# Optimization experiments

Measured on AMD Instinct MI355X. Metric: run time of the kernel, lower is better.

The kernel has to match this reference:

```python
import jax, jax.numpy as jnp
import numpy as np

B, H, W, Z = 4, 256, 256, 64
ITERATIONS = 8
EPSILON = 1e-06
CENTER = 6.0  # 7-point Laplacian diagonal


def _stencil(x):
    # x: [B, H, W, Z]; zero (Dirichlet) boundaries via padded shifts
    west = jnp.pad(x[:, :, :-1, :], ((0, 0), (0, 0), (1, 0), (0, 0)))
    east = jnp.pad(x[:, :, 1:, :], ((0, 0), (0, 0), (0, 1), (0, 0)))
    north = jnp.pad(x[:, :-1, :, :], ((0, 0), (1, 0), (0, 0), (0, 0)))
    south = jnp.pad(x[:, 1:, :, :], ((0, 0), (0, 1), (0, 0), (0, 0)))
    bottom = jnp.pad(x[:, :, :, :-1], ((0, 0), (0, 0), (0, 0), (1, 0)))
    top = jnp.pad(x[:, :, :, 1:], ((0, 0), (0, 0), (0, 0), (0, 1)))
    return CENTER * x - west - east - south - north - bottom - top


def _dot(a, b):
    # per-sample dot product, keepdims for scalar broadcast
    return jnp.sum(a * b, axis=(1, 2, 3), keepdims=True)


def setup_inputs() -> dict:
    key = jax.random.key(0)
    k1, k2, k3 = jax.random.split(key, 3)
    shape = (B, H, W, Z)
    return {
        "x": jax.random.normal(k1, shape, dtype=jnp.float32),
        "b": jax.random.normal(k2, shape, dtype=jnp.float32),
        "reference_sol": jax.random.normal(k3, shape, dtype=jnp.float32),
    }


def reference(x, b, reference_sol):
    r = b - _stencil(x)
    p = r
    rho = _dot(r, r)

    def body(carry, _):
        x, r, p, rho = carry
        w = _stencil(p)
        eta = _dot(p, w)
        alpha = rho / (eta + EPSILON)
        x = x + alpha * p
        r = r - alpha * w
        rho_next = _dot(r, r)
        beta = rho_next / (rho + EPSILON)
        p = r + beta * p
        return (x, r, p, rho_next), None

    (x, r, p, rho), _ = jax.lax.scan(body, (x, r, p, rho), None, length=ITERATIONS)

    diff = x - reference_sol
    loss = jnp.mean(diff * diff)
    max_error = jnp.max(jnp.abs(diff))
    residual_norm_sq = jnp.mean(rho)
    return (loss, x, max_error, residual_norm_sq)
```

## Files before the change

### kernel.cpp

```cpp
#include <hip/hip_runtime.h>

#define B_ 4
#define H_ 256
#define W_ 256
#define Z_ 64
#define NB_ (H_*W_*Z_)
#define N_  (B_*NB_)
#define ITER_ 8
#define EPS_ 1e-6f
#define SLOTS_ 64

#define RHO_OFF   0
#define ETA_OFF   ((ITER_+1)*B_*SLOTS_)
#define LOSS_OFF  (ETA_OFF + ITER_*B_*SLOTS_)
#define MAXE_OFF  (LOSS_OFF + SLOTS_)
#define SCAL_FLOATS (MAXE_OFF + SLOTS_)

struct F8 { float4 a, b; };

__device__ __forceinline__ float wsum(float v){
  v += __shfl_xor(v,32); v += __shfl_xor(v,16); v += __shfl_xor(v,8);
  v += __shfl_xor(v,4);  v += __shfl_xor(v,2);  v += __shfl_xor(v,1);
  return v;
}
__device__ __forceinline__ float wmaxr(float v){
  v = fmaxf(v,__shfl_xor(v,32)); v = fmaxf(v,__shfl_xor(v,16));
  v = fmaxf(v,__shfl_xor(v,8));  v = fmaxf(v,__shfl_xor(v,4));
  v = fmaxf(v,__shfl_xor(v,2));  v = fmaxf(v,__shfl_xor(v,1));
  return v;
}
__device__ __forceinline__ float read_sum(const float* s){
  return wsum(s[threadIdx.x & 63]);
}
__device__ __forceinline__ void block_atomic_sum(float v, float* dst, float* lds){
  v = wsum(v);
  int wid = threadIdx.x >> 6, lane = threadIdx.x & 63;
  if (lane == 0) lds[wid] = v;
  __syncthreads();
  if (threadIdx.x == 0) atomicAdd(dst, lds[0]+lds[1]+lds[2]+lds[3]);
}

__device__ __forceinline__ float4 ld4(const float* p){ return *(const float4*)p; }

__device__ __forceinline__ void sten_core(const F8& c, const F8& wm, const F8& wp,
                                          const F8& hm, const F8& hp,
                                          float zl, float zr, F8& st)
{
  st.a.x = 6.f*c.a.x - wm.a.x - wp.a.x - hm.a.x - hp.a.x - zl     - c.a.y;
  st.a.y = 6.f*c.a.y - wm.a.y - wp.a.y - hm.a.y - hp.a.y - c.a.x  - c.a.z;
  st.a.z = 6.f*c.a.z - wm.a.z - wp.a.z - hm.a.z - hp.a.z - c.a.y  - c.a.w;
  st.a.w = 6.f*c.a.w - wm.a.w - wp.a.w - hm.a.w - hp.a.w - c.a.z  - c.b.x;
  st.b.x = 6.f*c.b.x - wm.b.x - wp.b.x - hm.b.x - hp.b.x - c.a.w  - c.b.y;
  st.b.y = 6.f*c.b.y - wm.b.y - wp.b.y - hm.b.y - hp.b.y - c.b.x  - c.b.z;
  st.b.z = 6.f*c.b.z - wm.b.z - wp.b.z - hm.b.z - hp.b.z - c.b.y  - c.b.w;
  st.b.w = 6.f*c.b.w - wm.b.w - wp.b.w - hm.b.w - hp.b.w - c.b.z  - zr;
}

__device__ __forceinline__ void stencil1(const float* __restrict__ a, int base,
                                         int w, int h, int zc, F8& c, F8& st)
{
  c.a = ld4(a+base); c.b = ld4(a+base+4);
  F8 zero; zero.a = make_float4(0,0,0,0); zero.b = zero.a;
  F8 wm = zero, wp = zero, hm = zero, hp = zero;
  if (w > 0)    { wm.a = ld4(a+base-Z_);    wm.b = ld4(a+base-Z_+4); }
  if (w < W_-1) { wp.a = ld4(a+base+Z_);    wp.b = ld4(a+base+Z_+4); }
  if (h > 0)    { hm.a = ld4(a+base-W_*Z_); hm.b = ld4(a+base-W_*Z_+4); }
  if (h < H_-1) { hp.a = ld4(a+base+W_*Z_); hp.b = ld4(a+base+W_*Z_+4); }
  float zl = (zc > 0) ? a[base-1] : 0.f;
  float zr = (zc < 7) ? a[base+8] : 0.f;
  sten_core(c, wm, wp, hm, hp, zl, zr, st);
}

__device__ __forceinline__ F8 comb8(const float* r, const float* p, float beta, int idx){
  F8 o;
  float4 ra = ld4(r+idx), rb = ld4(r+idx+4);
  float4 pa = ld4(p+idx), pb = ld4(p+idx+4);
  o.a.x = ra.x + beta*pa.x; o.a.y = ra.y + beta*pa.y;
  o.a.z = ra.z + beta*pa.z; o.a.w = ra.w + beta*pa.w;
  o.b.x = rb.x + beta*pb.x; o.b.y = rb.y + beta*pb.y;
  o.b.z = rb.z + beta*pb.z; o.b.w = rb.w + beta*pb.w;
  return o;
}
__device__ __forceinline__ void stencil2(const float* __restrict__ r,
                                         const float* __restrict__ p, float beta,
                                         int base, int w, int h, int zc,
                                         F8& c, F8& st)
{
  c = comb8(r,p,beta,base);
  F8 zero; zero.a = make_float4(0,0,0,0); zero.b = zero.a;
  F8 wm = zero, wp = zero, hm = zero, hp = zero;
  if (w > 0)    wm = comb8(r,p,beta,base-Z_);
  if (w < W_-1) wp = comb8(r,p,beta,base+Z_);
  if (h > 0)    hm = comb8(r,p,beta,base-W_*Z_);
  if (h < H_-1) hp = comb8(r,p,beta,base+W_*Z_);
  float zl = (zc > 0) ? r[base-1] + beta*p[base-1] : 0.f;
  float zr = (zc < 7) ? r[base+8] + beta*p[base+8] : 0.f;
  sten_core(c, wm, wp, hm, hp, zl, zr, st);
}

#define IDX_SETUP \
  const int zc = threadIdx.x & 7; \
  const int wl = threadIdx.x >> 3; \
  const int w  = blockIdx.x*32 + wl; \
  const int h  = blockIdx.y; \
  const int bb = blockIdx.z; \
  const int base = ((bb*H_ + h)*W_ + w)*Z_ + zc*8; \
  const int flat = (blockIdx.z*gridDim.y + blockIdx.y)*gridDim.x + blockIdx.x; \
  const int slot = flat & (SLOTS_-1);

__global__ __launch_bounds__(256) void k_init(const float* __restrict__ x,
                                              const float* __restrict__ b,
                                              float* __restrict__ r,
                                              float* scal)
{
  __shared__ float lds[4];
  IDX_SETUP
  F8 c, st;
  stencil1(x, base, w, h, zc, c, st);
  float4 b0 = ld4(b+base), b1 = ld4(b+base+4);
  F8 rv;
  rv.a = make_float4(b0.x-st.a.x, b0.y-st.a.y, b0.z-st.a.z, b0.w-st.a.w);
  rv.b = make_float4(b1.x-st.b.x, b1.y-st.b.y, b1.z-st.b.z, b1.w-st.b.w);
  *(float4*)(r+base)   = rv.a;
  *(float4*)(r+base+4) = rv.b;
  float rho = rv.a.x*rv.a.x + rv.a.y*rv.a.y + rv.a.z*rv.a.z + rv.a.w*rv.a.w
            + rv.b.x*rv.b.x + rv.b.y*rv.b.y + rv.b.z*rv.b.z + rv.b.w*rv.b.w;
  block_atomic_sum(rho, scal + RHO_OFF + (0*B_+bb)*SLOTS_ + slot, lds);
}

__global__ __launch_bounds__(256) void k_a0(const float* __restrict__ r,
                                            float* __restrict__ pnew,
                                            float* scal)
{
  __shared__ float lds[4];
  IDX_SETUP
  F8 c, st;
  stencil1(r, base, w, h, zc, c, st);
  *(float4*)(pnew+base)   = c.a;
  *(float4*)(pnew+base+4) = c.b;
  float eta = c.a.x*st.a.x + c.a.y*st.a.y + c.a.z*st.a.z + c.a.w*st.a.w
            + c.b.x*st.b.x + c.b.y*st.b.y + c.b.z*st.b.z + c.b.w*st.b.w;
  block_atomic_sum(eta, scal + ETA_OFF + (0*B_+bb)*SLOTS_ + slot, lds);
}

__global__ __launch_bounds__(256) void k_a(const float* __restrict__ r,
                                           const float* __restrict__ pold,
                                           float* __restrict__ pnew,
                                           float* scal, int it)
{
  __shared__ float lds[4];
  IDX_SETUP
  float num = read_sum(scal + RHO_OFF + (it*B_+bb)*SLOTS_);
  float den = read_sum(scal + RHO_OFF + ((it-1)*B_+bb)*SLOTS_);
  float beta = num / (den + EPS_);
  F8 c, st;
  stencil2(r, pold, beta, base, w, h, zc, c, st);
  *(float4*)(pnew+base)   = c.a;
  *(float4*)(pnew+base+4) = c.b;
  float eta = c.a.x*st.a.x + c.a.y*st.a.y + c.a.z*st.a.z + c.a.w*st.a.w
            + c.b.x*st.b.x + c.b.y*st.b.y + c.b.z*st.b.z + c.b.w*st.b.w;
  block_atomic_sum(eta, scal + ETA_OFF + (it*B_+bb)*SLOTS_ + slot, lds);
}

__global__ __launch_bounds__(256) void k_b(float* __restrict__ x,
                                           float* __restrict__ r,
                                           const float* __restrict__ p,
                                           float* scal, int it)
{
  __shared__ float lds[4];
  IDX_SETUP
  float num = read_sum(scal + RHO_OFF + (it*B_+bb)*SLOTS_);
  float den = read_sum(scal + ETA_OFF + (it*B_+bb)*SLOTS_);
  float alpha = num / (den + EPS_);
  F8 c, st;
  stencil1(p, base, w, h, zc, c, st);
  float4 x0 = ld4(x+base), x1 = ld4(x+base+4);
  x0.x += alpha*c.a.x; x0.y += alpha*c.a.y; x0.z += alpha*c.a.z; x0.w += alpha*c.a.w;
  x1.x += alpha*c.b.x; x1.y += alpha*c.b.y; x1.z += alpha*c.b.z; x1.w += alpha*c.b.w;
  *(float4*)(x+base)   = x0;
  *(float4*)(x+base+4) = x1;
  float4 r0 = ld4(r+base), r1 = ld4(r+base+4);
  r0.x -= alpha*st.a.x; r0.y -= alpha*st.a.y; r0.z -= alpha*st.a.z; r0.w -= alpha*st.a.w;
  r1.x -= alpha*st.b.x; r1.y -= alpha*st.b.y; r1.z -= alpha*st.b.z; r1.w -= alpha*st.b.w;
  *(float4*)(r+base)   = r0;
  *(float4*)(r+base+4) = r1;
  float rho = r0.x*r0.x + r0.y*r0.y + r0.z*r0.z + r0.w*r0.w
            + r1.x*r1.x + r1.y*r1.y + r1.z*r1.z + r1.w*r1.w;
  block_atomic_sum(rho, scal + RHO_OFF + ((it+1)*B_+bb)*SLOTS_ + slot, lds);
}

__global__ __launch_bounds__(256) void k_b_fin(const float* __restrict__ x,
                                               const float* __restrict__ r,
                                               const float* __restrict__ p,
                                               const float* __restrict__ ref,
                                               float* __restrict__ out,
                                               float* scal, int it)
{
  __shared__ float xs[2048];
  __shared__ float lds[12];
  IDX_SETUP
  float num = read_sum(scal + RHO_OFF + (it*B_+bb)*SLOTS_);
  float den = read_sum(scal + ETA_OFF + (it*B_+bb)*SLOTS_);
  float alpha = num / (den + EPS_);
  F8 c, st;
  stencil1(p, base, w, h, zc, c, st);
  float4 x0 = ld4(x+base), x1 = ld4(x+base+4);
  x0.x += alpha*c.a.x; x0.y += alpha*c.a.y; x0.z += alpha*c.a.z; x0.w += alpha*c.a.w;
  x1.x += alpha*c.b.x; x1.y += alpha*c.b.y; x1.z += alpha*c.b.z; x1.w += alpha*c.b.w;
  float4 r0 = ld4(r+base), r1 = ld4(r+base+4);
  r0.x -= alpha*st.a.x; r0.y -= alpha*st.a.y; r0.z -= alpha*st.a.z; r0.w -= alpha*st.a.w;
  r1.x -= alpha*st.b.x; r1.y -= alpha*st.b.y; r1.z -= alpha*st.b.z; r1.w -= alpha*st.b.w;
  float rho = r0.x*r0.x + r0.y*r0.y + r0.z*r0.z + r0.w*r0.w
            + r1.x*r1.x + r1.y*r1.y + r1.z*r1.z + r1.w*r1.w;

  const int t = threadIdx.x;
  xs[t*8+0] = x0.x; xs[t*8+1] = x0.y; xs[t*8+2] = x0.z; xs[t*8+3] = x0.w;
  xs[t*8+4] = x1.x; xs[t*8+5] = x1.y; xs[t*8+6] = x1.z; xs[t*8+7] = x1.w;

  float4 f0 = ld4(ref+base), f1 = ld4(ref+base+4);
  float d0 = x0.x-f0.x, d1 = x0.y-f0.y, d2 = x0.z-f0.z, d3 = x0.w-f0.w;
  float d4 = x1.x-f1.x, d5 = x1.y-f1.y, d6 = x1.z-f1.z, d7 = x1.w-f1.w;
  float loss = d0*d0+d1*d1+d2*d2+d3*d3+d4*d4+d5*d5+d6*d6+d7*d7;
  float me = fmaxf(fmaxf(fmaxf(fabsf(d0),fabsf(d1)),fmaxf(fabsf(d2),fabsf(d3))),
                   fmaxf(fmaxf(fabsf(d4),fabsf(d5)),fmaxf(fabsf(d6),fabsf(d7))));

  float rs = wsum(rho), ls = wsum(loss), ms = wmaxr(me);
  int wid = t >> 6, lane = t & 63;
  if (lane == 0) { lds[wid] = rs; lds[4+wid] = ls; lds[8+wid] = ms; }
  __syncthreads();
  if (t == 0) {
    atomicAdd(scal + RHO_OFF + ((it+1)*B_+bb)*SLOTS_ + slot, lds[0]+lds[1]+lds[2]+lds[3]);
    atomicAdd(scal + LOSS_OFF + slot, lds[4]+lds[5]+lds[6]+lds[7]);
    float bm = fmaxf(fmaxf(lds[8],lds[9]), fmaxf(lds[10],lds[11]));
    atomicMax((unsigned int*)(scal + MAXE_OFF) + slot, __float_as_uint(bm));
  }

  const int S = flat * 2048;
  #pragma unroll
  for (int c2 = 0; c2 < 2; ++c2) {
    int q = t + 256*c2;
    if (q < 511) {
      float4 v = make_float4(xs[3+4*q], xs[4+4*q], xs[5+4*q], xs[6+4*q]);
      *(float4*)(out + S + 4 + 4*q) = v;
    } else if (q == 511) {
      out[S+1] = xs[0]; out[S+2] = xs[1]; out[S+3] = xs[2];
      out[S+2048] = xs[2047];
    }
  }
}

__global__ __launch_bounds__(64) void k_scal(const float* scal, float* out)
{
  int lane = threadIdx.x;
  float loss = wsum(scal[LOSS_OFF + lane]);
  float me   = wmaxr(__uint_as_float(((const unsigned int*)scal)[MAXE_OFF + lane]));
  float rho_sum = 0.f;
  for (int bb = 0; bb < B_; ++bb)
    rho_sum += wsum(scal[RHO_OFF + (ITER_*B_+bb)*SLOTS_ + lane]);
  if (lane == 0) {
    out[0]      = loss / (float)N_;
    out[1+N_]   = me;
    out[2+N_]   = rho_sum / (float)B_;
  }
}

extern "C" void kernel_launch(void* const* d_in, const int* in_sizes, int n_in,
                              void* d_out, int out_size, void* d_ws, size_t ws_size,
                              hipStream_t stream) {
  float* x         = (float*)d_in[0];
  const float* b   = (const float*)d_in[1];
  const float* ref = (const float*)d_in[2];
  float* out       = (float*)d_out;

  float* r  = (float*)d_ws;
  float* p0 = r + N_;
  float* p1;
  float* scal;
  size_t need3 = ((size_t)3*N_ + SCAL_FLOATS) * sizeof(float);
  if (ws_size >= need3) {
    p1   = p0 + N_;
    scal = p1 + N_;
  } else {
    p1   = (float*)d_out;
    scal = p0 + N_;
  }

  (void)hipMemsetAsync(scal, 0, SCAL_FLOATS*sizeof(float), stream);

  dim3 grid(W_/32, H_, B_), blk(256);
  k_init<<<grid, blk, 0, stream>>>(x, b, r, scal);

  float* pa = p1;
  float* pb = p0;
  for (int it = 0; it < ITER_; ++it) {
    if (it == 0)
      k_a0<<<grid, blk, 0, stream>>>(r, pa, scal);
    else
      k_a<<<grid, blk, 0, stream>>>(r, pb, pa, scal, it);
    if (it < ITER_-1)
      k_b<<<grid, blk, 0, stream>>>(x, r, pa, scal, it);
    else
      k_b_fin<<<grid, blk, 0, stream>>>(x, r, pa, ref, out, scal, it);
    float* t = pa; pa = pb; pb = t;
  }

  k_scal<<<1, 64, 0, stream>>>(scal, out);
}
```

Baseline: 1.096 ms.

## Defer x updates by storing all search directions and reconstructing x at end

When the workspace can hold eight p vectors, the per-iteration update kernel no longer reads and writes x. Each iteration's p is kept in its own buffer. A final k_recon kernel sums x0 plus alpha_j times p_j, then computes loss and max error and writes the output with nontemporal stores. This removes a read and a write of x in every iteration, at the cost of eight extra reads in the final pass and a much larger workspace; whether it runs depends on the workspace size provided.

```diff
diff --git a/kernel.cpp b/kernel.cpp
--- a/kernel.cpp
+++ b/kernel.cpp
@@ -17,6 +17,7 @@
 #define SCAL_FLOATS (MAXE_OFF + SLOTS_)
 
 struct F8 { float4 a, b; };
+typedef float v4f __attribute__((ext_vector_type(4)));
 
 __device__ __forceinline__ float wsum(float v){
   v += __shfl_xor(v,32); v += __shfl_xor(v,16); v += __shfl_xor(v,8);
@@ -160,6 +161,100 @@
   float eta = c.a.x*st.a.x + c.a.y*st.a.y + c.a.z*st.a.z + c.a.w*st.a.w
             + c.b.x*st.b.x + c.b.y*st.b.y + c.b.z*st.b.z + c.b.w*st.b.w;
   block_atomic_sum(eta, scal + ETA_OFF + (it*B_+bb)*SLOTS_ + slot, lds);
+}
+
+__global__ __launch_bounds__(256) void k_bh(float* __restrict__ r,
+                                            const float* __restrict__ p,
+                                            float* scal, int it)
+{
+  __shared__ float lds[4];
+  IDX_SETUP
+  float num = read_sum(scal + RHO_OFF + (it*B_+bb)*SLOTS_);
+  float den = read_sum(scal + ETA_OFF + (it*B_+bb)*SLOTS_);
+  float alpha = num / (den + EPS_);
+  F8 c, st;
+  stencil1(p, base, w, h, zc, c, st);
+  float4 r0 = ld4(r+base), r1 = ld4(r+base+4);
+  r0.x -= alpha*st.a.x; r0.y -= alpha*st.a.y; r0.z -= alpha*st.a.z; r0.w -= alpha*st.a.w;
+  r1.x -= alpha*st.b.x; r1.y -= alpha*st.b.y; r1.z -= alpha*st.b.z; r1.w -= alpha*st.b.w;
+  *(float4*)(r+base)   = r0;
+  *(float4*)(r+base+4) = r1;
+  float rho = r0.x*r0.x + r0.y*r0.y + r0.z*r0.z + r0.w*r0.w
+            + r1.x*r1.x + r1.y*r1.y + r1.z*r1.z + r1.w*r1.w;
+  block_atomic_sum(rho, scal + RHO_OFF + ((it+1)*B_+bb)*SLOTS_ + slot, lds);
+}
+
+__global__ __launch_bounds__(256) void k_bh_last(const float* __restrict__ r,
+                                                 const float* __restrict__ p,
+                                                 float* scal, int it)
+{
+  __shared__ float lds[4];
+  IDX_SETUP
+  float num = read_sum(scal + RHO_OFF + (it*B_+bb)*SLOTS_);
+  float den = read_sum(scal + ETA_OFF + (it*B_+bb)*SLOTS_);
+  float alpha = num / (den + EPS_);
+  F8 c, st;
+  stencil1(p, base, w, h, zc, c, st);
+  float4 r0 = ld4(r+base), r1 = ld4(r+base+4);
+  r0.x -= alpha*st.a.x; r0.y -= alpha*st.a.y; r0.z -= alpha*st.a.z; r0.w -= alpha*st.a.w;
+  r1.x -= alpha*st.b.x; r1.y -= alpha*st.b.y; r1.z -= alpha*st.b.z; r1.w -= alpha*st.b.w;
+  float rho = r0.x*r0.x + r0.y*r0.y + r0.z*r0.z + r0.w*r0.w
+            + r1.x*r1.x + r1.y*r1.y + r1.z*r1.z + r1.w*r1.w;
+  block_atomic_sum(rho, scal + RHO_OFF + ((it+1)*B_+bb)*SLOTS_ + slot, lds);
+}
+
+__global__ __launch_bounds__(256) void k_recon(const float* __restrict__ x0,
+                                               const float* __restrict__ ref,
+                                               const float* __restrict__ ph,
+                                               float* __restrict__ out,
+                                               float* scal)
+{
+  __shared__ float bnd[256];
+  __shared__ float lds[8];
+  IDX_SETUP
+  (void)slot;
+  float4 a0 = ld4(x0+base), a1 = ld4(x0+base+4);
+  float v0=a0.x, v1=a0.y, v2=a0.z, v3=a0.w, v4=a1.x, v5=a1.y, v6=a1.z, v7=a1.w;
+  #pragma unroll
+  for (int j = 0; j < ITER_; ++j) {
+    float num = read_sum(scal + RHO_OFF + (j*B_+bb)*SLOTS_);
+    float den = read_sum(scal + ETA_OFF + (j*B_+bb)*SLOTS_);
+    float alpha = num / (den + EPS_);
+    const float* pj = ph + (size_t)j*N_;
+    float4 q0 = ld4(pj+base), q1 = ld4(pj+base+4);
+    v0 += alpha*q0.x; v1 += alpha*q0.y; v2 += alpha*q0.z; v3 += alpha*q0.w;
+    v4 += alpha*q1.x; v5 += alpha*q1.y; v6 += alpha*q1.z; v7 += alpha*q1.w;
+  }
+
+  float4 f0 = ld4(ref+base), f1 = ld4(ref+base+4);
+  float d0 = v0-f0.x, d1 = v1-f0.y, d2 = v2-f0.z, d3 = v3-f0.w;
+  float d4 = v4-f1.x, d5 = v5-f1.y, d6 = v6-f1.z, d7 = v7-f1.w;
+  float loss = d0*d0+d1*d1+d2*d2+d3*d3+d4*d4+d5*d5+d6*d6+d7*d7;
+  float me = fmaxf(fmaxf(fmaxf(fabsf(d0),fabsf(d1)),fmaxf(fabsf(d2),fabsf(d3))),
+                   fmaxf(fmaxf(fabsf(d4),fabsf(d5)),fmaxf(fabsf(d6),fabsf(d7))));
+  float ls = wsum(loss), ms = wmaxr(me);
+  const int t = threadIdx.x;
+  int wid = t >> 6, lane = t & 63;
+  if (lane == 0) { lds[wid] = ls; lds[4+wid] = ms; }
+
+  bnd[t] = v7;
+  __syncthreads();
+  if (t == 0) {
+    atomicAdd(scal + LOSS_OFF + (flat & (SLOTS_-1)), lds[0]+lds[1]+lds[2]+lds[3]);
+    float bm = fmaxf(fmaxf(lds[4],lds[5]), fmaxf(lds[6],lds[7]));
+    atomicMax((unsigned int*)(scal + MAXE_OFF) + (flat & (SLOTS_-1)), __float_as_uint(bm));
+  }
+
+  const int S = flat * 2048;
+  v4f chB = { v3, v4, v5, v6 };
+  __builtin_nontemporal_store(chB, (v4f*)(out + S + 8*t + 4));
+  if (t > 0) {
+    v4f chA = { bnd[t-1], v0, v1, v2 };
+    __builtin_nontemporal_store(chA, (v4f*)(out + S + 8*t));
+  } else {
+    out[S+1] = v0; out[S+2] = v1; out[S+3] = v2;
+  }
+  if (t == 255) out[S+2048] = v7;
 }
 
 __global__ __launch_bounds__(256) void k_b(float* __restrict__ x,
@@ -212,18 +307,15 @@
   r1.x -= alpha*st.b.x; r1.y -= alpha*st.b.y; r1.z -= alpha*st.b.z; r1.w -= alpha*st.b.w;
   float rho = r0.x*r0.x + r0.y*r0.y + r0.z*r0.z + r0.w*r0.w
             + r1.x*r1.x + r1.y*r1.y + r1.z*r1.z + r1.w*r1.w;
-
   const int t = threadIdx.x;
   xs[t*8+0] = x0.x; xs[t*8+1] = x0.y; xs[t*8+2] = x0.z; xs[t*8+3] = x0.w;
   xs[t*8+4] = x1.x; xs[t*8+5] = x1.y; xs[t*8+6] = x1.z; xs[t*8+7] = x1.w;
-
   float4 f0 = ld4(ref+base), f1 = ld4(ref+base+4);
   float d0 = x0.x-f0.x, d1 = x0.y-f0.y, d2 = x0.z-f0.z, d3 = x0.w-f0.w;
   float d4 = x1.x-f1.x, d5 = x1.y-f1.y, d6 = x1.z-f1.z, d7 = x1.w-f1.w;
   float loss = d0*d0+d1*d1+d2*d2+d3*d3+d4*d4+d5*d5+d6*d6+d7*d7;
   float me = fmaxf(fmaxf(fmaxf(fabsf(d0),fabsf(d1)),fmaxf(fabsf(d2),fabsf(d3))),
                    fmaxf(fmaxf(fabsf(d4),fabsf(d5)),fmaxf(fabsf(d6),fabsf(d7))));
-
   float rs = wsum(rho), ls = wsum(loss), ms = wmaxr(me);
   int wid = t >> 6, lane = t & 63;
   if (lane == 0) { lds[wid] = rs; lds[4+wid] = ls; lds[8+wid] = ms; }
@@ -234,7 +326,6 @@
     float bm = fmaxf(fmaxf(lds[8],lds[9]), fmaxf(lds[10],lds[11]));
     atomicMax((unsigned int*)(scal + MAXE_OFF) + slot, __float_as_uint(bm));
   }
-
   const int S = flat * 2048;
   #pragma unroll
   for (int c2 = 0; c2 < 2; ++c2) {
@@ -272,37 +363,47 @@
   const float* ref = (const float*)d_in[2];
   float* out       = (float*)d_out;
 
-  float* r  = (float*)d_ws;
-  float* p0 = r + N_;
-  float* p1;
-  float* scal;
-  size_t need3 = ((size_t)3*N_ + SCAL_FLOATS) * sizeof(float);
-  if (ws_size >= need3) {
-    p1   = p0 + N_;
-    scal = p1 + N_;
+  dim3 grid(W_/32, H_, B_), blk(256);
+
+  size_t needH = ((size_t)9*N_ + SCAL_FLOATS) * sizeof(float);
+  if (ws_size >= needH) {
+    float* r    = (float*)d_ws;
+    float* ph   = r + N_;
+    float* scal = ph + (size_t)8*N_;
+    (void)hipMemsetAsync(scal, 0, SCAL_FLOATS*sizeof(float), stream);
+
+    k_init<<<grid, blk, 0, stream>>>(x, b, r, scal);
+    k_a0<<<grid, blk, 0, stream>>>(r, ph, scal);
+    for (int it = 0; it < ITER_; ++it) {
+      if (it < ITER_-1) {
+        k_bh<<<grid, blk, 0, stream>>>(r, ph + (size_t)it*N_, scal, it);
+        k_a<<<grid, blk, 0, stream>>>(r, ph + (size_t)it*N_, ph + (size_t)(it+1)*N_, scal, it+1);
+      } else {
+        k_bh_last<<<grid, blk, 0, stream>>>(r, ph + (size_t)it*N_, scal, it);
+      }
+    }
+    k_recon<<<grid, blk, 0, stream>>>(x, ref, ph, out, scal);
+    k_scal<<<1, 64, 0, stream>>>(scal, out);
   } else {
-    p1   = (float*)d_out;
-    scal = p0 + N_;
-  }
-
-  (void)hipMemsetAsync(scal, 0, SCAL_FLOATS*sizeof(float), stream);
-
-  dim3 grid(W_/32, H_, B_), blk(256);
-  k_init<<<grid, blk, 0, stream>>>(x, b, r, scal);
-
-  float* pa = p1;
-  float* pb = p0;
-  for (int it = 0; it < ITER_; ++it) {
-    if (it == 0)
-      k_a0<<<grid, blk, 0, stream>>>(r, pa, scal);
-    else
-      k_a<<<grid, blk, 0, stream>>>(r, pb, pa, scal, it);
-    if (it < ITER_-1)
-      k_b<<<grid, blk, 0, stream>>>(x, r, pa, scal, it);
-    else
-      k_b_fin<<<grid, blk, 0, stream>>>(x, r, pa, ref, out, scal, it);
-    float* t = pa; pa = pb; pb = t;
-  }
-
-  k_scal<<<1, 64, 0, stream>>>(scal, out);
-}
+    float* r  = (float*)d_ws;
+    float* p0 = r + N_;
+    float* p1;
+    float* scal;
+    size_t need3 = ((size_t)3*N_ + SCAL_FLOATS) * sizeof(float);
+    if (ws_size >= need3) { p1 = p0 + N_; scal = p1 + N_; }
+    else                  { p1 = (float*)d_out; scal = p0 + N_; }
+    (void)hipMemsetAsync(scal, 0, SCAL_FLOATS*sizeof(float), stream);
+
+    k_init<<<grid, blk, 0, stream>>>(x, b, r, scal);
+    float* pa = p1;
+    float* pb = p0;
+    for (int it = 0; it < ITER_; ++it) {
+      if (it == 0) k_a0<<<grid, blk, 0, stream>>>(r, pa, scal);
+      else         k_a<<<grid, blk, 0, stream>>>(r, pb, pa, scal, it);
+      if (it < ITER_-1) k_b<<<grid, blk, 0, stream>>>(x, r, pa, scal, it);
+      else              k_b_fin<<<grid, blk, 0, stream>>>(x, r, pa, ref, out, scal, it);
+      float* t = pa; pa = pb; pb = t;
+    }
+    k_scal<<<1, 64, 0, stream>>>(scal, out);
+  }
+}
```

Result: no change. 1.096 ms (+0.0%).
